# Kernel optimization log

Hardware: AMD Instinct MI355X
Metric: run time of the kernel (lower is better)

The kernel has to match this reference:

```python
import jax
import jax.numpy as jnp
import numpy as np
from jax import lax

GAMMA = 0.99  # cfg.offline_gamma
TAU = 0.95    # cfg.tau (GAE lambda)
T = 4_194_304  # trajectory length (many episodes concatenated, separated by mask=0)


def setup_inputs() -> dict:
    key = jax.random.key(0)
    k1, k2, k3, k4 = jax.random.split(key, 4)
    rewards = jax.random.normal(k1, (T, 1), dtype=jnp.float32)
    values = jax.random.normal(k2, (T, 1), dtype=jnp.float32)        # critic.get_max_value(states)
    next_values = jax.random.normal(k3, (T, 1), dtype=jnp.float32)   # critic.get_max_value(next_states) (bootstrap=True)
    masks = jax.random.randint(k4, (T, 1), 0, 2).astype(jnp.int32)   # 1 = non-terminal, 0 = episode end
    return {"rewards": rewards, "values": values, "next_values": next_values, "masks": masks}


def reference(rewards, values, next_values, masks):
    """Faithful translation of A2C.get_phi's reversed loop as a single lax.scan.

    returns[i]    = r[i] + gamma * (prev_return * m[i] + (1 - m[i]) * next_values[i])
    deltas[i]     = r[i] + gamma * prev_value * m[i] - values[i]
    advantages[i] = deltas[i] + gamma * tau * prev_advantage * m[i]
    with prev_* taken from step i+1 (zeros past the end).
    """
    m = masks.astype(rewards.dtype)  # [T,1]

    def step(carry, xs):
        prev_ret, prev_val, prev_adv = carry  # each [1]
        r, v, nv, mm = xs                     # each [1]
        ret = r + GAMMA * (prev_ret * mm + (1.0 - mm) * nv)
        delta = r + GAMMA * prev_val * mm - v
        adv = delta + GAMMA * TAU * prev_adv * mm
        return (ret, v, adv), (adv, ret)

    zero = jnp.zeros((1,), dtype=rewards.dtype)
    init = (zero, zero, zero)
    _, (advantages, returns) = lax.scan(
        step, init, (rewards, values, next_values, m), reverse=True
    )
    return advantages, returns  # each [T,1]
```

## Files before the change

kernel.cpp:

```cpp
#include <hip/hip_runtime.h>

#define GAMMA 0.99f
#define TAU   0.95f
#define GTAU  (GAMMA * TAU)

constexpr int WSEQ   = 4;
constexpr int WCHUNK = 64 * WSEQ;
constexpr int BLK    = 256;

typedef float fx4 __attribute__((ext_vector_type(4)));

__device__ __forceinline__ void post_compose(float& A, float& B, float rA, float rB) {
    B = fmaf(A, rB, B);
    A *= rA;
}
__device__ __forceinline__ void pre_compose(float& A, float& B, float lA, float lB) {
    B = fmaf(lA, B, lB);
    A *= lA;
}

__global__ __launch_bounds__(BLK) void k_wave(
    const float* __restrict__ r, const float* __restrict__ v,
    const float* __restrict__ nv, const int* __restrict__ m,
    float* __restrict__ out_adv, float* __restrict__ out_ret, int T, int nchunk)
{
    const int  lane  = threadIdx.x & 63;
    const int  w     = threadIdx.x >> 6;
    const int  chunk = (int)blockIdx.x * 4 + w;
    if (chunk >= nchunk) return;

    const long base = (long)chunk * WCHUNK + (long)lane * WSEQ;
    const long p    = (long)(chunk + 1) * WCHUNK;

    float pm = 0.f, pr = 0.f, pv = 0.f, pv1 = 0.f, pnv = 0.f;
    if (p < (long)T) {
        long i = p + lane;
        if (i < (long)T) {
            pm  = (float)m[i];
            pr  = r[i];
            pv  = v[i];
            pv1 = (i + 1 < (long)T) ? v[i + 1] : 0.f;
            pnv = nv[i];
        }
    }

    float delta[WSEQ], dd[WSEQ];
    unsigned vbits = 0, mbits = 0;
    float Aa = 1.f, Ba = 0.f, Ar = 1.f, Br = 0.f;
    const bool full = (p <= (long)T);

    if (full) {
        vbits = 0xFu;
        float4 r4 = *(const float4*)(r  + base);
        float4 v4 = *(const float4*)(v  + base);
        float4 n4 = *(const float4*)(nv + base);
        int4   m4 = *(const int4*)  (m  + base);
        float vhi   = __shfl(pv, 0);
        float vnext = __shfl_down(v4.x, 1);
        if (lane == 63) vnext = vhi;

        float rr[4]  = {r4.x, r4.y, r4.z, r4.w};
        float vv[5]  = {v4.x, v4.y, v4.z, v4.w, vnext};
        float nn[4]  = {n4.x, n4.y, n4.z, n4.w};
        float fmv[4] = {(float)m4.x, (float)m4.y, (float)m4.z, (float)m4.w};
        #pragma unroll
        for (int i = WSEQ - 1; i >= 0; --i) {
            if (fmv[i] != 0.f) mbits |= (1u << i);
            delta[i] = rr[i] + GAMMA * fmv[i] * vv[i+1] - vv[i];
            dd[i]    = rr[i] + GAMMA * (1.f - fmv[i]) * nn[i];
            pre_compose(Aa, Ba, GTAU  * fmv[i], delta[i]);
            pre_compose(Ar, Br, GAMMA * fmv[i], dd[i]);
        }
    } else {
        #pragma unroll
        for (int ii = 0; ii < WSEQ; ++ii) {
            int i = WSEQ - 1 - ii;
            long idx = base + i;
            bool val = idx < (long)T;
            float rr  = val ? r[idx]  : 0.f;
            float vv0 = val ? v[idx]  : 0.f;
            float vv1 = (idx + 1 < (long)T) ? v[idx + 1] : 0.f;
            float nn  = val ? nv[idx] : 0.f;
            float fmv = val ? (float)m[idx] : 0.f;
            if (val) vbits |= (1u << i);
            if (val && fmv != 0.f) mbits |= (1u << i);
            delta[i] = val ? (rr + GAMMA * fmv * vv1 - vv0) : 0.f;
            dd[i]    = val ? (rr + GAMMA * (1.f - fmv) * nn) : 0.f;
            pre_compose(Aa, Ba, val ? GTAU * fmv  : 1.f, delta[i]);
            pre_compose(Ar, Br, val ? GAMMA * fmv : 1.f, dd[i]);
        }
    }

    #pragma unroll
    for (int st = 1; st < 64; st <<= 1) {
        float oAa = __shfl_down(Aa, st);
        float oBa = __shfl_down(Ba, st);
        float oAr = __shfl_down(Ar, st);
        float oBr = __shfl_down(Br, st);
        if (lane + st < 64) {
            post_compose(Aa, Ba, oAa, oBa);
            post_compose(Ar, Br, oAr, oBr);
        }
    }
    float eAa = __shfl_down(Aa, 1);
    float eBa = __shfl_down(Ba, 1);
    float eAr = __shfl_down(Ar, 1);
    float eBr = __shfl_down(Br, 1);
    if (lane == 63) { eAa=1.f; eBa=0.f; eAr=1.f; eBr=0.f; }

    float cbA = 0.f, cbR = 0.f;
    if (p < (long)T) {
        float MAa, MBa, MAr, MBr;
        {
            long i = p + lane;
            bool have = i < (long)T;
            float aA=1.f, aB=0.f, rA_=1.f, rB_=0.f;
            if (have) {
                aA  = GTAU * pm;
                aB  = pr + GAMMA * pm * pv1 - pv;
                rA_ = GAMMA * pm;
                rB_ = pr + GAMMA * (1.f - pm) * pnv;
            }
            bool term = (!have) || (pm == 0.f);
            unsigned long long bz = __ballot(term);
            #pragma unroll
            for (int st = 1; st < 64; st <<= 1) {
                float oAa = __shfl_down(aA,  st);
                float oBa = __shfl_down(aB,  st);
                float oAr = __shfl_down(rA_, st);
                float oBr = __shfl_down(rB_, st);
                if (lane + st < 64) {
                    post_compose(aA,  aB,  oAa, oBa);
                    post_compose(rA_, rB_, oAr, oBr);
                }
            }
            MAa = __shfl(aA, 0);  MBa = __shfl(aB, 0);
            MAr = __shfl(rA_, 0); MBr = __shfl(rB_, 0);
            if (bz == 0ull) {
                for (long jb = p + 64; ; jb += 64) {
                    long i2 = jb + lane;
                    bool have2 = i2 < (long)T;
                    float aA2=1.f, aB2=0.f, rA2=1.f, rB2=0.f;
                    float mi = 0.f;
                    if (have2) {
                        mi = (float)m[i2];
                        float ri  = r[i2];
                        float vi  = v[i2];
                        float vi1 = (i2 + 1 < (long)T) ? v[i2 + 1] : 0.f;
                        float nvi = nv[i2];
                        aA2 = GTAU * mi;
                        aB2 = ri + GAMMA * mi * vi1 - vi;
                        rA2 = GAMMA * mi;
                        rB2 = ri + GAMMA * (1.f - mi) * nvi;
                    }
                    bool term2 = (!have2) || (mi == 0.f);
                    unsigned long long bz2 = __ballot(term2);
                    #pragma unroll
                    for (int st = 1; st < 64; st <<= 1) {
                        float oAa = __shfl_down(aA2, st);
                        float oBa = __shfl_down(aB2, st);
                        float oAr = __shfl_down(rA2, st);
                        float oBr = __shfl_down(rB2, st);
                        if (lane + st < 64) {
                            post_compose(aA2, aB2, oAa, oBa);
                            post_compose(rA2, rB2, oAr, oBr);
                        }
                    }
                    float bAa = __shfl(aA2, 0), bBa = __shfl(aB2, 0);
                    float bAr = __shfl(rA2, 0), bBr = __shfl(rB2, 0);
                    post_compose(MAa, MBa, bAa, bBa);
                    post_compose(MAr, MBr, bAr, bBr);
                    if (bz2 != 0ull) break;
                }
            }
        }
        cbA = MBa;
        cbR = MBr;
    }

    float xa = fmaf(eAa, cbA, eBa);
    float xr = fmaf(eAr, cbR, eBr);

    if (full) {
        float ta[4], tr[4];
        #pragma unroll
        for (int i = WSEQ - 1; i >= 0; --i) {
            float a  = (mbits >> i & 1u) ? GTAU  : 0.f;
            float cc = (mbits >> i & 1u) ? GAMMA : 0.f;
            xa = fmaf(a,  xa, delta[i]);
            xr = fmaf(cc, xr, dd[i]);
            ta[i] = xa; tr[i] = xr;
        }
        fx4 va = {ta[0], ta[1], ta[2], ta[3]};
        fx4 vr = {tr[0], tr[1], tr[2], tr[3]};
        __builtin_nontemporal_store(va, (fx4*)(out_adv + base));
        __builtin_nontemporal_store(vr, (fx4*)(out_ret + base));
    } else {
        #pragma unroll
        for (int i = WSEQ - 1; i >= 0; --i) {
            bool val = (vbits >> i) & 1u;
            float a  = val ? ((mbits >> i & 1u) ? GTAU  : 0.f) : 1.f;
            float cc = val ? ((mbits >> i & 1u) ? GAMMA : 0.f) : 1.f;
            xa = fmaf(a,  xa, delta[i]);
            xr = fmaf(cc, xr, dd[i]);
            if (base + i < (long)T) {
                out_adv[base + i] = xa;
                out_ret[base + i] = xr;
            }
        }
    }
}

extern "C" void kernel_launch(void* const* d_in, const int* in_sizes, int n_in,
                              void* d_out, int out_size, void* d_ws, size_t ws_size,
                              hipStream_t stream) {
    const float* r  = (const float*)d_in[0];
    const float* v  = (const float*)d_in[1];
    const float* nv = (const float*)d_in[2];
    const int*   m  = (const int*)d_in[3];
    const int T = in_sizes[0];
    const int nchunk = (T + WCHUNK - 1) / WCHUNK;
    const int nblk   = (nchunk + 3) / 4;

    float* out_adv = (float*)d_out;
    float* out_ret = (float*)d_out + T;

    k_wave<<<nblk, BLK, 0, stream>>>(r, v, nv, m, out_adv, out_ret, T, nchunk);
}
```

Before: 22.40 us.

## Process two 256-element tiles per wave to amortize lookahead carry resolution

Each wave now covers two consecutive 256-element tiles instead of one, scanning both locally and chaining the carry from the later tile into the earlier one with a broadcast from lane 0. This halves the number of waves, and with it the per-wave lookahead scan over the following chunk that resolves the incoming carry, which is redundant work. The cost is more registers and more serial work per wave, less parallelism, and a launch bound hint of 4 that may constrain register allocation.

```diff
diff --git a/kernel.cpp b/kernel.cpp
--- a/kernel.cpp
+++ b/kernel.cpp
@@ -4,8 +4,9 @@
 #define TAU   0.95f
 #define GTAU  (GAMMA * TAU)
 
-constexpr int WSEQ   = 4;
-constexpr int WCHUNK = 64 * WSEQ;
+constexpr int TSEQ   = 4;
+constexpr int TILE   = 64 * TSEQ;
+constexpr int WCHUNK = 2 * TILE;
 constexpr int BLK    = 256;
 
 typedef float fx4 __attribute__((ext_vector_type(4)));
@@ -19,7 +20,29 @@
     A *= lA;
 }
 
-__global__ __launch_bounds__(BLK) void k_wave(
+__device__ __forceinline__ void scan_excl(
+    int lane, float& Aa, float& Ba, float& Ar, float& Br,
+    float& eAa, float& eBa, float& eAr, float& eBr)
+{
+    #pragma unroll
+    for (int st = 1; st < 64; st <<= 1) {
+        float oAa = __shfl_down(Aa, st);
+        float oBa = __shfl_down(Ba, st);
+        float oAr = __shfl_down(Ar, st);
+        float oBr = __shfl_down(Br, st);
+        if (lane + st < 64) {
+            post_compose(Aa, Ba, oAa, oBa);
+            post_compose(Ar, Br, oAr, oBr);
+        }
+    }
+    eAa = __shfl_down(Aa, 1);
+    eBa = __shfl_down(Ba, 1);
+    eAr = __shfl_down(Ar, 1);
+    eBr = __shfl_down(Br, 1);
+    if (lane == 63) { eAa = 1.f; eBa = 0.f; eAr = 1.f; eBr = 0.f; }
+}
+
+__global__ __launch_bounds__(BLK, 4) void k_wave2(
     const float* __restrict__ r, const float* __restrict__ v,
     const float* __restrict__ nv, const int* __restrict__ m,
     float* __restrict__ out_adv, float* __restrict__ out_ret, int T, int nchunk)
@@ -29,8 +52,10 @@
     const int  chunk = (int)blockIdx.x * 4 + w;
     if (chunk >= nchunk) return;
 
-    const long base = (long)chunk * WCHUNK + (long)lane * WSEQ;
-    const long p    = (long)(chunk + 1) * WCHUNK;
+    const long cstart = (long)chunk * WCHUNK;
+    const long baseA  = cstart + (long)lane * TSEQ;
+    const long baseB  = cstart + TILE + (long)lane * TSEQ;
+    const long p      = cstart + WCHUNK;
 
     float pm = 0.f, pr = 0.f, pv = 0.f, pv1 = 0.f, pnv = 0.f;
     if (p < (long)T) {
@@ -44,69 +69,99 @@
         }
     }
 
-    float delta[WSEQ], dd[WSEQ];
-    unsigned vbits = 0, mbits = 0;
-    float Aa = 1.f, Ba = 0.f, Ar = 1.f, Br = 0.f;
     const bool full = (p <= (long)T);
 
+    float dA[TSEQ], ddA[TSEQ], dB[TSEQ], ddB[TSEQ];
+    unsigned vbA = 0, mbA = 0, vbB = 0, mbB = 0;
+    float AaA=1.f, BaA=0.f, ArA=1.f, BrA=0.f;
+    float AaB=1.f, BaB=0.f, ArB=1.f, BrB=0.f;
+
     if (full) {
-        vbits = 0xFu;
-        float4 r4 = *(const float4*)(r  + base);
-        float4 v4 = *(const float4*)(v  + base);
-        float4 n4 = *(const float4*)(nv + base);
-        int4   m4 = *(const int4*)  (m  + base);
-        float vhi   = __shfl(pv, 0);
-        float vnext = __shfl_down(v4.x, 1);
-        if (lane == 63) vnext = vhi;
-
-        float rr[4]  = {r4.x, r4.y, r4.z, r4.w};
-        float vv[5]  = {v4.x, v4.y, v4.z, v4.w, vnext};
-        float nn[4]  = {n4.x, n4.y, n4.z, n4.w};
-        float fmv[4] = {(float)m4.x, (float)m4.y, (float)m4.z, (float)m4.w};
-        #pragma unroll
-        for (int i = WSEQ - 1; i >= 0; --i) {
-            if (fmv[i] != 0.f) mbits |= (1u << i);
-            delta[i] = rr[i] + GAMMA * fmv[i] * vv[i+1] - vv[i];
-            dd[i]    = rr[i] + GAMMA * (1.f - fmv[i]) * nn[i];
-            pre_compose(Aa, Ba, GTAU  * fmv[i], delta[i]);
-            pre_compose(Ar, Br, GAMMA * fmv[i], dd[i]);
+        vbA = 0xFu; vbB = 0xFu;
+        float4 r4a = *(const float4*)(r  + baseA);
+        float4 r4b = *(const float4*)(r  + baseB);
+        float4 v4a = *(const float4*)(v  + baseA);
+        float4 v4b = *(const float4*)(v  + baseB);
+        float4 n4a = *(const float4*)(nv + baseA);
+        float4 n4b = *(const float4*)(nv + baseB);
+        int4   m4a = *(const int4*)  (m  + baseA);
+        int4   m4b = *(const int4*)  (m  + baseB);
+
+        float vp  = __shfl(pv, 0);
+        float vb0 = __shfl(v4b.x, 0);
+        float vnB = __shfl_down(v4b.x, 1);
+        float vnA = __shfl_down(v4a.x, 1);
+        float vnextB = (lane == 63) ? vp  : vnB;
+        float vnextA = (lane == 63) ? vb0 : vnA;
+
+        {
+            float rr[4]  = {r4b.x, r4b.y, r4b.z, r4b.w};
+            float vv[5]  = {v4b.x, v4b.y, v4b.z, v4b.w, vnextB};
+            float nn[4]  = {n4b.x, n4b.y, n4b.z, n4b.w};
+            float fmv[4] = {(float)m4b.x, (float)m4b.y, (float)m4b.z, (float)m4b.w};
+            #pragma unroll
+            for (int i = TSEQ - 1; i >= 0; --i) {
+                if (fmv[i] != 0.f) mbB |= (1u << i);
+                dB[i]  = rr[i] + GAMMA * fmv[i] * vv[i+1] - vv[i];
+                ddB[i] = rr[i] + GAMMA * (1.f - fmv[i]) * nn[i];
+                pre_compose(AaB, BaB, GTAU  * fmv[i], dB[i]);
+                pre_compose(ArB, BrB, GAMMA * fmv[i], ddB[i]);
+            }
+        }
+        {
+            float rr[4]  = {r4a.x, r4a.y, r4a.z, r4a.w};
+            float vv[5]  = {v4a.x, v4a.y, v4a.z, v4a.w, vnextA};
+            float nn[4]  = {n4a.x, n4a.y, n4a.z, n4a.w};
+            float fmv[4] = {(float)m4a.x, (float)m4a.y, (float)m4a.z, (float)m4a.w};
+            #pragma unroll
+            for (int i = TSEQ - 1; i >= 0; --i) {
+                if (fmv[i] != 0.f) mbA |= (1u << i);
+                dA[i]  = rr[i] + GAMMA * fmv[i] * vv[i+1] - vv[i];
+                ddA[i] = rr[i] + GAMMA * (1.f - fmv[i]) * nn[i];
+                pre_compose(AaA, BaA, GTAU  * fmv[i], dA[i]);
+                pre_compose(ArA, BrA, GAMMA * fmv[i], ddA[i]);
+            }
         }
     } else {
         #pragma unroll
-        for (int ii = 0; ii < WSEQ; ++ii) {
-            int i = WSEQ - 1 - ii;
-            long idx = base + i;
+        for (int ii = 0; ii < TSEQ; ++ii) {
+            int i = TSEQ - 1 - ii;
+            long idx = baseB + i;
             bool val = idx < (long)T;
             float rr  = val ? r[idx]  : 0.f;
             float vv0 = val ? v[idx]  : 0.f;
             float vv1 = (idx + 1 < (long)T) ? v[idx + 1] : 0.f;
             float nn  = val ? nv[idx] : 0.f;
             float fmv = val ? (float)m[idx] : 0.f;
-            if (val) vbits |= (1u << i);
-            if (val && fmv != 0.f) mbits |= (1u << i);
-            delta[i] = val ? (rr + GAMMA * fmv * vv1 - vv0) : 0.f;
-            dd[i]    = val ? (rr + GAMMA * (1.f - fmv) * nn) : 0.f;
-            pre_compose(Aa, Ba, val ? GTAU * fmv  : 1.f, delta[i]);
-            pre_compose(Ar, Br, val ? GAMMA * fmv : 1.f, dd[i]);
-        }
-    }
-
-    #pragma unroll
-    for (int st = 1; st < 64; st <<= 1) {
-        float oAa = __shfl_down(Aa, st);
-        float oBa = __shfl_down(Ba, st);
-        float oAr = __shfl_down(Ar, st);
-        float oBr = __shfl_down(Br, st);
-        if (lane + st < 64) {
-            post_compose(Aa, Ba, oAa, oBa);
-            post_compose(Ar, Br, oAr, oBr);
-        }
-    }
-    float eAa = __shfl_down(Aa, 1);
-    float eBa = __shfl_down(Ba, 1);
-    float eAr = __shfl_down(Ar, 1);
-    float eBr = __shfl_down(Br, 1);
-    if (lane == 63) { eAa=1.f; eBa=0.f; eAr=1.f; eBr=0.f; }
+            if (val) vbB |= (1u << i);
+            if (val && fmv != 0.f) mbB |= (1u << i);
+            dB[i]  = val ? (rr + GAMMA * fmv * vv1 - vv0) : 0.f;
+            ddB[i] = val ? (rr + GAMMA * (1.f - fmv) * nn) : 0.f;
+            pre_compose(AaB, BaB, val ? GTAU * fmv  : 1.f, dB[i]);
+            pre_compose(ArB, BrB, val ? GAMMA * fmv : 1.f, ddB[i]);
+        }
+        #pragma unroll
+        for (int ii = 0; ii < TSEQ; ++ii) {
+            int i = TSEQ - 1 - ii;
+            long idx = baseA + i;
+            bool val = idx < (long)T;
+            float rr  = val ? r[idx]  : 0.f;
+            float vv0 = val ? v[idx]  : 0.f;
+            float vv1 = (idx + 1 < (long)T) ? v[idx + 1] : 0.f;
+            float nn  = val ? nv[idx] : 0.f;
+            float fmv = val ? (float)m[idx] : 0.f;
+            if (val) vbA |= (1u << i);
+            if (val && fmv != 0.f) mbA |= (1u << i);
+            dA[i]  = val ? (rr + GAMMA * fmv * vv1 - vv0) : 0.f;
+            ddA[i] = val ? (rr + GAMMA * (1.f - fmv) * nn) : 0.f;
+            pre_compose(AaA, BaA, val ? GTAU * fmv  : 1.f, dA[i]);
+            pre_compose(ArA, BrA, val ? GAMMA * fmv : 1.f, ddA[i]);
+        }
+    }
+
+    float eAaB, eBaB, eArB, eBrB, eAaA, eBaA, eArA, eBrA;
+    scan_excl(lane, AaB, BaB, ArB, BrB, eAaB, eBaB, eArB, eBrB);
+    scan_excl(lane, AaA, BaA, ArA, BrA, eAaA, eBaA, eArA, eBrA);
 
     float cbA = 0.f, cbR = 0.f;
     if (p < (long)T) {
@@ -178,34 +233,69 @@
         cbR = MBr;
     }
 
-    float xa = fmaf(eAa, cbA, eBa);
-    float xr = fmaf(eAr, cbR, eBr);
+    float xa = fmaf(eAaB, cbA, eBaB);
+    float xr = fmaf(eArB, cbR, eBrB);
 
     if (full) {
         float ta[4], tr[4];
         #pragma unroll
-        for (int i = WSEQ - 1; i >= 0; --i) {
-            float a  = (mbits >> i & 1u) ? GTAU  : 0.f;
-            float cc = (mbits >> i & 1u) ? GAMMA : 0.f;
-            xa = fmaf(a,  xa, delta[i]);
-            xr = fmaf(cc, xr, dd[i]);
+        for (int i = TSEQ - 1; i >= 0; --i) {
+            float a  = (mbB >> i & 1u) ? GTAU  : 0.f;
+            float cc = (mbB >> i & 1u) ? GAMMA : 0.f;
+            xa = fmaf(a,  xa, dB[i]);
+            xr = fmaf(cc, xr, ddB[i]);
             ta[i] = xa; tr[i] = xr;
         }
         fx4 va = {ta[0], ta[1], ta[2], ta[3]};
         fx4 vr = {tr[0], tr[1], tr[2], tr[3]};
-        __builtin_nontemporal_store(va, (fx4*)(out_adv + base));
-        __builtin_nontemporal_store(vr, (fx4*)(out_ret + base));
+        __builtin_nontemporal_store(va, (fx4*)(out_adv + baseB));
+        __builtin_nontemporal_store(vr, (fx4*)(out_ret + baseB));
     } else {
         #pragma unroll
-        for (int i = WSEQ - 1; i >= 0; --i) {
-            bool val = (vbits >> i) & 1u;
-            float a  = val ? ((mbits >> i & 1u) ? GTAU  : 0.f) : 1.f;
-            float cc = val ? ((mbits >> i & 1u) ? GAMMA : 0.f) : 1.f;
-            xa = fmaf(a,  xa, delta[i]);
-            xr = fmaf(cc, xr, dd[i]);
-            if (base + i < (long)T) {
-                out_adv[base + i] = xa;
-                out_ret[base + i] = xr;
+        for (int i = TSEQ - 1; i >= 0; --i) {
+            bool val = (vbB >> i) & 1u;
+            float a  = val ? ((mbB >> i & 1u) ? GTAU  : 0.f) : 1.f;
+            float cc = val ? ((mbB >> i & 1u) ? GAMMA : 0.f) : 1.f;
+            xa = fmaf(a,  xa, dB[i]);
+            xr = fmaf(cc, xr, ddB[i]);
+            if (baseB + i < (long)T) {
+                out_adv[baseB + i] = xa;
+                out_ret[baseB + i] = xr;
+            }
+        }
+    }
+
+    float cbA2 = __shfl(xa, 0);
+    float cbR2 = __shfl(xr, 0);
+
+    xa = fmaf(eAaA, cbA2, eBaA);
+    xr = fmaf(eArA, cbR2, eBrA);
+
+    if (full) {
+        float ta[4], tr[4];
+        #pragma unroll
+        for (int i = TSEQ - 1; i >= 0; --i) {
+            float a  = (mbA >> i & 1u) ? GTAU  : 0.f;
+            float cc = (mbA >> i & 1u) ? GAMMA : 0.f;
+            xa = fmaf(a,  xa, dA[i]);
+            xr = fmaf(cc, xr, ddA[i]);
+            ta[i] = xa; tr[i] = xr;
+        }
+        fx4 va = {ta[0], ta[1], ta[2], ta[3]};
+        fx4 vr = {tr[0], tr[1], tr[2], tr[3]};
+        __builtin_nontemporal_store(va, (fx4*)(out_adv + baseA));
+        __builtin_nontemporal_store(vr, (fx4*)(out_ret + baseA));
+    } else {
+        #pragma unroll
+        for (int i = TSEQ - 1; i >= 0; --i) {
+            bool val = (vbA >> i) & 1u;
+            float a  = val ? ((mbA >> i & 1u) ? GTAU  : 0.f) : 1.f;
+            float cc = val ? ((mbA >> i & 1u) ? GAMMA : 0.f) : 1.f;
+            xa = fmaf(a,  xa, dA[i]);
+            xr = fmaf(cc, xr, ddA[i]);
+            if (baseA + i < (long)T) {
+                out_adv[baseA + i] = xa;
+                out_ret[baseA + i] = xr;
             }
         }
     }
@@ -225,5 +315,5 @@
     float* out_adv = (float*)d_out;
     float* out_ret = (float*)d_out + T;
 
-    k_wave<<<nblk, BLK, 0, stream>>>(r, v, nv, m, out_adv, out_ret, T, nchunk);
-}
+    k_wave2<<<nblk, BLK, 0, stream>>>(r, v, nv, m, out_adv, out_ret, T, nchunk);
+}
```

After: 22.51 us. Within noise of the previous version (+0.5%).
